# Performance work log

Measured on AMD Instinct MI355X. Metric: run time of the kernel, lower is better.

The kernel has to match this reference:

```python
import jax, jax.numpy as jnp
import numpy as np

B, S, HIDDEN = 2, 2048, 2048
NUM_HEADS, NUM_KV_HEADS, HEAD_DIM = 16, 4, 128
Q_SIZE = NUM_HEADS * HEAD_DIM          # 2048
KV_SIZE = NUM_KV_HEADS * HEAD_DIM      # 512
ROPE_THETA = 10000.0
NEG = -1e30


def setup_inputs() -> dict:
    key = jax.random.key(0)
    k1, k2, k3 = jax.random.split(key, 3)
    hidden_states = jax.random.normal(k1, (B, S, HIDDEN), jnp.float32)
    w_qkv = jax.random.normal(k2, (HIDDEN, Q_SIZE + 2 * KV_SIZE), jnp.float32) / np.sqrt(HIDDEN)
    w_o = jax.random.normal(k3, (Q_SIZE, HIDDEN), jnp.float32) / np.sqrt(Q_SIZE)
    positions = jnp.broadcast_to(jnp.arange(S, dtype=jnp.int32), (B, S))
    return {"positions": positions, "hidden_states": hidden_states,
            "w_qkv": w_qkv, "w_o": w_o}


def _rope(x, positions):
    # x: [B, S, H, D], neox-style rotate-half rope over full head_dim
    d = x.shape[-1]
    inv_freq = 1.0 / (ROPE_THETA ** (jnp.arange(0, d, 2, dtype=jnp.float32) / d))
    ang = positions[..., None].astype(jnp.float32) * inv_freq      # [B, S, D/2]
    cos = jnp.cos(ang)[:, :, None, :]
    sin = jnp.sin(ang)[:, :, None, :]
    x1, x2 = jnp.split(x, 2, axis=-1)
    return jnp.concatenate([x1 * cos - x2 * sin, x2 * cos + x1 * sin], axis=-1)


def reference(positions, hidden_states, w_qkv, w_o):
    qkv = jnp.einsum('bsh,ho->bso', hidden_states, w_qkv)
    q, k, v = jnp.split(qkv, [Q_SIZE, Q_SIZE + KV_SIZE], axis=-1)
    q = q.reshape(B, S, NUM_HEADS, HEAD_DIM)
    k = k.reshape(B, S, NUM_KV_HEADS, HEAD_DIM)
    v = v.reshape(B, S, NUM_KV_HEADS, HEAD_DIM)
    q = _rope(q, positions)
    k = _rope(k, positions)
    rep = NUM_HEADS // NUM_KV_HEADS
    k = jnp.repeat(k, rep, axis=2)   # GQA expand -> [B, S, NUM_HEADS, D]
    v = jnp.repeat(v, rep, axis=2)
    scale = HEAD_DIM ** -0.5
    scores = jnp.einsum('bqhd,bkhd->bhqk', q, k) * scale   # [B, H, S, S]
    causal = jnp.tril(jnp.ones((S, S), dtype=bool))
    scores = jnp.where(causal, scores, NEG)
    probs = jax.nn.softmax(scores, axis=-1)
    attn = jnp.einsum('bhqk,bkhd->bqhd', probs, v).reshape(B, S, Q_SIZE)
    return jnp.einsum('bsq,qh->bsh', attn, w_o)
```

## Files before the change

kernel.cpp:

```cpp
#include <hip/hip_runtime.h>
#include <hip/hip_bf16.h>
#include <stdint.h>

#define BDIM 2
#define SDIM 2048
#define HID 2048
#define NH 16
#define NKV 4
#define HD 128
#define QSZ 2048
#define KVSZ 512
#define QKVW 3072
#define TOK (BDIM*SDIM)

typedef __attribute__((ext_vector_type(8))) short bf16x8;
typedef __attribute__((ext_vector_type(4))) float f32x4;
typedef __attribute__((ext_vector_type(16))) float f32x16;

__device__ __forceinline__ short f2bf(float f) {
  return (short)__bfloat16_as_ushort(__float2bfloat16(f));
}

__device__ __forceinline__ float exp2_fast(float x) {
  float r;
  asm("v_exp_f32 %0, %1" : "=v"(r) : "v"(x));
  return r;
}

__device__ __forceinline__ void sincos_rev(float rev, float* sn, float* cs) {
  float fr, s, c;
  asm("v_fract_f32 %0, %1" : "=v"(fr) : "v"(rev));
  asm("v_sin_f32 %0, %1" : "=v"(s) : "v"(fr));
  asm("v_cos_f32 %0, %1" : "=v"(c) : "v"(fr));
  *sn = s; *cs = c;
}

__device__ __forceinline__ int xcd_swz(int orig, int nwg) {
  int cpx = nwg >> 3;
  return (orig & 7) * cpx + (orig >> 3);
}

__device__ __forceinline__ void gload_lds16(const void* g, void* lds) {
  __builtin_amdgcn_global_load_lds(
      (const __attribute__((address_space(1))) void*)g,
      (__attribute__((address_space(3))) void*)lds, 16, 0, 0);
}

__global__ __launch_bounds__(256) void k_prep(const float* __restrict__ hidden,
                                              const float* __restrict__ w_qkv,
                                              const float* __restrict__ w_o,
                                              short* __restrict__ X,
                                              short* __restrict__ WqkvT,
                                              short* __restrict__ WoT) {
  __shared__ short tile[64][65];
  const int bid = blockIdx.x;
  const int t = threadIdx.x;
  if (bid < 8192) {
    int i = (bid * 256 + t) * 4;
    float4 v = *(const float4*)(hidden + i);
    short4 o; o.x = f2bf(v.x); o.y = f2bf(v.y); o.z = f2bf(v.z); o.w = f2bf(v.w);
    *(short4*)(X + i) = o;
    return;
  }
  const float* in; short* out; int R, C, bx, by;
  if (bid < 9728) {
    int tt = bid - 8192; in = w_qkv; out = WqkvT; R = HID; C = QKVW;
    bx = tt % 48; by = tt / 48;
  } else {
    int tt = bid - 9728; in = w_o; out = WoT; R = QSZ; C = HID;
    bx = tt & 31; by = tt >> 5;
  }
  int k0 = by * 64, n0 = bx * 64;
#pragma unroll
  for (int i = 0; i < 16; ++i) {
    int idx = i * 256 + t;
    int kk = idx >> 6, nn = idx & 63;
    tile[kk][nn] = f2bf(in[(size_t)(k0 + kk) * C + n0 + nn]);
  }
  __syncthreads();
#pragma unroll
  for (int i = 0; i < 16; ++i) {
    int idx = i * 256 + t;
    int nn = idx >> 6, kk = idx & 63;
    out[(size_t)(n0 + nn) * R + k0 + kk] = tile[kk][nn];
  }
}

__global__ __launch_bounds__(256) void k_gemm_bf16(const short* __restrict__ A,
                                                   const short* __restrict__ Bt,
                                                   float* __restrict__ C,
                                                   int M, int N, int K) {
  __shared__ char lds[128 * 32 * 2 * 2];
  char* As = lds;
  char* Bs = lds + 8192;
  const int tid = threadIdx.x;
  const int w = tid >> 6, l = tid & 63;
  const int lq = l & 15, g = l >> 4;
  const int nx = N >> 7;
  const int bid = xcd_swz(blockIdx.x, nx * (M >> 7));
  const int m0 = (bid / nx) * 128, n0 = (bid % nx) * 128;
  const int wm = (w >> 1) * 64, wn = (w & 1) * 64;
  f32x4 acc[4][4] = {};

  const int nk = K >> 5;
  for (int kt = 0; kt < nk; ++kt) {
    const int k0 = kt * 32;
#pragma unroll
    for (int i = 0; i < 2; ++i) {
      int ch = (w + 4 * i) * 64 + l;
      int r = ch >> 2, cc = ch & 3;
      int gc = cc ^ ((r >> 1) & 3);
      gload_lds16(A + (size_t)(m0 + r) * K + k0 + gc * 8, As + (w + 4 * i) * 1024);
      gload_lds16(Bt + (size_t)(n0 + r) * K + k0 + gc * 8, Bs + (w + 4 * i) * 1024);
    }
    __syncthreads();
    bf16x8 af[4], bfr[4];
#pragma unroll
    for (int mi = 0; mi < 4; ++mi) {
      int row = wm + mi * 16 + lq;
      af[mi] = *(const bf16x8*)(As + row * 64 + ((g ^ ((row >> 1) & 3)) * 16));
    }
#pragma unroll
    for (int ni = 0; ni < 4; ++ni) {
      int row = wn + ni * 16 + lq;
      bfr[ni] = *(const bf16x8*)(Bs + row * 64 + ((g ^ ((row >> 1) & 3)) * 16));
    }
#pragma unroll
    for (int mi = 0; mi < 4; ++mi)
#pragma unroll
      for (int ni = 0; ni < 4; ++ni)
        acc[mi][ni] = __builtin_amdgcn_mfma_f32_16x16x32_bf16(af[mi], bfr[ni],
                                                              acc[mi][ni], 0, 0, 0);
    __syncthreads();
  }
#pragma unroll
  for (int mi = 0; mi < 4; ++mi)
#pragma unroll
    for (int ni = 0; ni < 4; ++ni)
#pragma unroll
      for (int r = 0; r < 4; ++r) {
        int row = m0 + wm + mi * 16 + 4 * g + r;
        int col = n0 + wn + ni * 16 + lq;
        C[(size_t)row * N + col] = acc[mi][ni][r];
      }
}

__global__ __launch_bounds__(256) void k_gemm_qkv_rope(const short* __restrict__ A,
                                                       const short* __restrict__ Bt,
                                                       const int* __restrict__ pos,
                                                       short* __restrict__ Qh,
                                                       short* __restrict__ Kh,
                                                       short* __restrict__ VT) {
  __shared__ char lds[128 * 32 * 2 * 2];
  char* As = lds;
  char* Bs = lds + 8192;
  const int tid = threadIdx.x;
  const int w = tid >> 6, l = tid & 63;
  const int lq = l & 15, g = l >> 4;
  const int bid = xcd_swz(blockIdx.x, (QKVW >> 7) * (TOK >> 7));
  const int hx = bid % (QKVW >> 7);
  const int m0 = (bid / (QKVW >> 7)) * 128, n0 = hx * 128;
  const int K = HID;
  f32x4 acc[2][8] = {};

  const int nk = K >> 5;
  for (int kt = 0; kt < nk; ++kt) {
    const int k0 = kt * 32;
#pragma unroll
    for (int i = 0; i < 2; ++i) {
      int ch = (w + 4 * i) * 64 + l;
      int r = ch >> 2, cc = ch & 3;
      int gc = cc ^ ((r >> 1) & 3);
      gload_lds16(A + (size_t)(m0 + r) * K + k0 + gc * 8, As + (w + 4 * i) * 1024);
      gload_lds16(Bt + (size_t)(n0 + r) * K + k0 + gc * 8, Bs + (w + 4 * i) * 1024);
    }
    __syncthreads();
    bf16x8 af[2], bfr[8];
#pragma unroll
    for (int mi = 0; mi < 2; ++mi) {
      int row = w * 32 + mi * 16 + lq;
      af[mi] = *(const bf16x8*)(As + row * 64 + ((g ^ ((row >> 1) & 3)) * 16));
    }
#pragma unroll
    for (int ni = 0; ni < 8; ++ni) {
      int row = ni * 16 + lq;
      bfr[ni] = *(const bf16x8*)(Bs + row * 64 + ((g ^ ((row >> 1) & 3)) * 16));
    }
#pragma unroll
    for (int mi = 0; mi < 2; ++mi)
#pragma unroll
      for (int ni = 0; ni < 8; ++ni)
        acc[mi][ni] = __builtin_amdgcn_mfma_f32_16x16x32_bf16(af[mi], bfr[ni],
                                                              acc[mi][ni], 0, 0, 0);
    __syncthreads();
  }

  const int b = m0 >> 11;
  if (hx < 20) {
    const float qscale = 0.12751743920f;
    const float sc = (hx < 16) ? qscale : 1.0f;
    short* dst = (hx < 16) ? (Qh + (size_t)(b * NH + hx) * SDIM * HD)
                           : (Kh + (size_t)(b * NKV + (hx - 16)) * SDIM * HD);
    float invf[4];
#pragma unroll
    for (int ni = 0; ni < 4; ++ni)
      invf[ni] = 0.15915494309f *
                 exp2_fast(-(float)(ni * 16 + lq) * (13.287712379549449f / 64.0f));
#pragma unroll
    for (int mi = 0; mi < 2; ++mi)
#pragma unroll
      for (int r = 0; r < 4; ++r) {
        int row = m0 + w * 32 + mi * 16 + 4 * g + r;
        int s = row & (SDIM - 1);
        float p = (float)pos[row];
        size_t hb = (size_t)s * HD;
#pragma unroll
        for (int ni = 0; ni < 4; ++ni) {
          float sn, cs;
          sincos_rev(p * invf[ni], &sn, &cs);
          float x1 = acc[mi][ni][r], x2 = acc[mi][ni + 4][r];
          dst[hb + ni * 16 + lq] = f2bf((x1 * cs - x2 * sn) * sc);
          dst[hb + ni * 16 + lq + 64] = f2bf((x2 * cs + x1 * sn) * sc);
        }
      }
  } else {
    const int hv = hx - 20;
    const int s00 = (m0 & (SDIM - 1)) + w * 32;
#pragma unroll
    for (int mi = 0; mi < 2; ++mi)
#pragma unroll
      for (int ni = 0; ni < 8; ++ni) {
        int d = ni * 16 + lq;
        int s0 = s00 + mi * 16 + 4 * g;
        size_t vb = ((size_t)(b * NKV + hv) * HD + d) * SDIM + s0;
        short4 ov;
        ov.x = f2bf(acc[mi][ni][0]); ov.y = f2bf(acc[mi][ni][1]);
        ov.z = f2bf(acc[mi][ni][2]); ov.w = f2bf(acc[mi][ni][3]);
        *(short4*)(VT + vb) = ov;
      }
  }
}

__global__ __launch_bounds__(256, 2) void k_attn(const short* __restrict__ Qh,
                                                 const short* __restrict__ Kh,
                                                 const short* __restrict__ VT,
                                                 short* __restrict__ attn, int S) {
  __shared__ char lds[2][32768];
  const int tid = threadIdx.x;
  const int w = tid >> 6, l = tid & 63;
  const int l31 = l & 31, hi = l >> 5;
  const int nqc = S / 128;
  const int bid = blockIdx.x;
  const int b = bid / (NH * nqc);
  const int rem = bid % (NH * nqc);
  const int h = rem / nqc;
  const int qc = nqc - 1 - (rem % nqc);
  const int q0 = qc * 128 + w * 32;
  const int kvh = h >> 2;
  const short* Qp = Qh + (size_t)(b * NH + h) * S * HD;
  const short* Kp = Kh + (size_t)(b * NKV + kvh) * S * HD;
  const short* Vp = VT + (size_t)(b * NKV + kvh) * HD * S;

  bf16x8 qf[8];
#pragma unroll
  for (int kc = 0; kc < 8; ++kc)
    qf[kc] = *(const bf16x8*)(Qp + (size_t)(q0 + l31) * HD + kc * 16 + hi * 8);

  f32x16 o[4] = {};
  float mrun = -1e30f, lrun = 0.f;
  const int qabs = q0 + l31;
  const int ntu = qc * 2 + 2;

#define STAGE(bufi, c0_)                                                          \
  {                                                                               \
    char* Kb = lds[bufi];                                                         \
    char* Vb = lds[bufi] + 16384;                                                 \
    _Pragma("unroll")                                                             \
    for (int i = 0; i < 4; ++i) {                                                 \
      int id = (i * 4 + w) * 64 + l;                                              \
      int kr = id >> 4, c16 = id & 15;                                            \
      gload_lds16(Kp + (size_t)((c0_) + kr) * HD + ((c16 ^ (kr & 15)) * 8),       \
                  Kb + (i * 4 + w) * 1024);                                       \
      int vr = id >> 3, c8 = id & 7;                                              \
      gload_lds16(Vp + (size_t)vr * S + (c0_) + ((c8 ^ (vr & 7)) * 8),            \
                  Vb + (i * 4 + w) * 1024);                                       \
    }                                                                             \
  }

  STAGE(0, 0);
  asm volatile("s_waitcnt vmcnt(0)" ::: "memory");
  __builtin_amdgcn_s_barrier();

  for (int c = 0; c < ntu; ++c) {
    const int c0 = c * 64;
    const int cur = c & 1;
    if (c + 1 < ntu) STAGE(cur ^ 1, c0 + 64);
    const char* Ks = lds[cur];
    const char* Vs = lds[cur] + 16384;

    f32x16 st[2];
    __builtin_amdgcn_s_setprio(1);
#pragma unroll
    for (int tt = 0; tt < 2; ++tt) {
      f32x16 s = {};
#pragma unroll
      for (int kc = 0; kc < 8; ++kc) {
        int kr = tt * 32 + l31;
        bf16x8 kf = *(const bf16x8*)(Ks + kr * 256 + (((kc * 2 + hi) ^ (l31 & 15)) * 16));
        s = __builtin_amdgcn_mfma_f32_32x32x16_bf16(kf, qf[kc], s, 0, 0, 0);
      }
      st[tt] = s;
    }
    __builtin_amdgcn_s_setprio(0);
    float tmax = -1e30f;
    if (c0 + 64 <= q0) {
#pragma unroll
      for (int tt = 0; tt < 2; ++tt)
#pragma unroll
        for (int r = 0; r < 16; ++r) tmax = fmaxf(tmax, st[tt][r]);
    } else {
#pragma unroll
      for (int tt = 0; tt < 2; ++tt)
#pragma unroll
        for (int r = 0; r < 16; ++r) {
          int kv = c0 + tt * 32 + (r & 3) + 8 * (r >> 2) + 4 * hi;
          float sv = (kv <= qabs) ? st[tt][r] : -1e30f;
          st[tt][r] = sv;
          tmax = fmaxf(tmax, sv);
        }
    }
    tmax = fmaxf(tmax, __shfl_xor(tmax, 32));
    if (!__all(tmax - mrun <= 8.0f)) {
      float mnew = fmaxf(mrun, tmax);
      float fac = exp2_fast(mrun - mnew);
      lrun *= fac;
#pragma unroll
      for (int d0 = 0; d0 < 4; ++d0) o[d0] = o[d0] * fac;
      mrun = mnew;
    }
    float sum = 0.f;
#pragma unroll
    for (int tt = 0; tt < 2; ++tt)
#pragma unroll
      for (int r = 0; r < 16; ++r) {
        float e = exp2_fast(st[tt][r] - mrun);
        st[tt][r] = e;
        sum += e;
      }
    sum += __shfl_xor(sum, 32);
    lrun += sum;
    __builtin_amdgcn_s_setprio(1);
#pragma unroll
    for (int j = 0; j < 4; ++j) {
      const int tt = j >> 1, kc = j & 1;
      uint32_t W0 = (uint32_t)(uint16_t)f2bf(st[tt][8 * kc + 0]) |
                    ((uint32_t)(uint16_t)f2bf(st[tt][8 * kc + 1]) << 16);
      uint32_t W1 = (uint32_t)(uint16_t)f2bf(st[tt][8 * kc + 2]) |
                    ((uint32_t)(uint16_t)f2bf(st[tt][8 * kc + 3]) << 16);
      uint32_t W2 = (uint32_t)(uint16_t)f2bf(st[tt][8 * kc + 4]) |
                    ((uint32_t)(uint16_t)f2bf(st[tt][8 * kc + 5]) << 16);
      uint32_t W3 = (uint32_t)(uint16_t)f2bf(st[tt][8 * kc + 6]) |
                    ((uint32_t)(uint16_t)f2bf(st[tt][8 * kc + 7]) << 16);
      uint32_t Y0 = __shfl_xor(hi ? W0 : W2, 32);
      uint32_t Y1 = __shfl_xor(hi ? W1 : W3, 32);
      union { uint32_t u[4]; bf16x8 v; } pu;
      pu.u[0] = hi ? Y0 : W0;
      pu.u[1] = hi ? Y1 : W1;
      pu.u[2] = hi ? W2 : Y0;
      pu.u[3] = hi ? W3 : Y1;
#pragma unroll
      for (int d0 = 0; d0 < 4; ++d0) {
        int vr = d0 * 32 + l31;
        bf16x8 vf = *(const bf16x8*)(Vs + vr * 128 + (((j * 2 + hi) ^ (vr & 7)) * 16));
        o[d0] = __builtin_amdgcn_mfma_f32_32x32x16_bf16(vf, pu.v, o[d0], 0, 0, 0);
      }
    }
    __builtin_amdgcn_s_setprio(0);
    asm volatile("s_waitcnt vmcnt(0)" ::: "memory");
    __builtin_amdgcn_s_barrier();
  }
#undef STAGE
  float inv = 1.0f / lrun;
  size_t rowb = (size_t)(b * S + q0 + l31) * QSZ + h * HD;
#pragma unroll
  for (int d0 = 0; d0 < 4; ++d0)
#pragma unroll
    for (int gq = 0; gq < 4; ++gq) {
      short4 ov;
      ov.x = f2bf(o[d0][4 * gq + 0] * inv);
      ov.y = f2bf(o[d0][4 * gq + 1] * inv);
      ov.z = f2bf(o[d0][4 * gq + 2] * inv);
      ov.w = f2bf(o[d0][4 * gq + 3] * inv);
      *(short4*)(attn + rowb + d0 * 32 + 8 * gq + 4 * hi) = ov;
    }
}

extern "C" void kernel_launch(void* const* d_in, const int* in_sizes, int n_in,
                              void* d_out, int out_size, void* d_ws, size_t ws_size,
                              hipStream_t stream) {
  const int* positions = (const int*)d_in[0];
  const float* hidden = (const float*)d_in[1];
  const float* w_qkv = (const float*)d_in[2];
  const float* w_o = (const float*)d_in[3];
  float* out = (float*)d_out;

  char* ws = (char*)d_ws;
  short* X     = (short*)(ws);
  short* WqkvT = (short*)(ws + 16777216);
  short* WoT   = (short*)(ws + 29360128);
  short* Qh    = (short*)(ws + 88080384);
  short* Kh    = (short*)(ws + 104857600);
  short* VT    = (short*)(ws + 109051904);
  short* ATT   = (short*)(ws + 113246208);

  k_prep<<<10752, 256, 0, stream>>>(hidden, w_qkv, w_o, X, WqkvT, WoT);
  k_gemm_qkv_rope<<<(QKVW / 128) * (TOK / 128), 256, 0, stream>>>(X, WqkvT, positions,
                                                                  Qh, Kh, VT);
  k_attn<<<BDIM * NH * (SDIM / 128), 256, 0, stream>>>(Qh, Kh, VT, ATT, SDIM);
  k_gemm_bf16<<<(HID / 128) * (TOK / 128), 256, 0, stream>>>(ATT, WoT, out, TOK, HID, QSZ);
}
```

Measured before the change: 217.6 us.

## Restructure attention so one block serves four GQA heads with 16x16 MFMA tiles

Each attention block now handles one KV head and 16 query rows, with its four waves covering the four query heads that share that KV head, so each staged K/V tile is reused across heads. The kernel moves from 32x32x16 to 16x16x32 MFMA, uses 32-key chunks with smaller LDS buffers, and passes P through a per-wave LDS scratch instead of cross-lane shuffles. Launch bounds rise to 4 blocks per CU and the grid doubles. In exchange, each block covers fewer query rows, so K/V traffic per query and the number of barriers per key grow.

New measurement: 234.1 us. +7.6%, slower.

```diff
diff --git a/kernel.cpp b/kernel.cpp
--- a/kernel.cpp
+++ b/kernel.cpp
@@ -241,48 +241,50 @@
   }
 }
 
-__global__ __launch_bounds__(256, 2) void k_attn(const short* __restrict__ Qh,
+__global__ __launch_bounds__(256, 4) void k_attn(const short* __restrict__ Qh,
                                                  const short* __restrict__ Kh,
                                                  const short* __restrict__ VT,
                                                  short* __restrict__ attn, int S) {
-  __shared__ char lds[2][32768];
+  __shared__ char lds[2][16384];
+  __shared__ __align__(16) char plds[4][1280];
   const int tid = threadIdx.x;
   const int w = tid >> 6, l = tid & 63;
-  const int l31 = l & 31, hi = l >> 5;
-  const int nqc = S / 128;
+  const int lq = l & 15, g = l >> 4;
+  const int ntc = S / 16;
   const int bid = blockIdx.x;
-  const int b = bid / (NH * nqc);
-  const int rem = bid % (NH * nqc);
-  const int h = rem / nqc;
-  const int qc = nqc - 1 - (rem % nqc);
-  const int q0 = qc * 128 + w * 32;
-  const int kvh = h >> 2;
+  const int b = bid / (NKV * ntc);
+  const int rem = bid % (NKV * ntc);
+  const int kvh = rem / ntc;
+  const int tc = ntc - 1 - (rem % ntc);
+  const int q0 = tc * 16;
+  const int h = kvh * 4 + w;
   const short* Qp = Qh + (size_t)(b * NH + h) * S * HD;
   const short* Kp = Kh + (size_t)(b * NKV + kvh) * S * HD;
   const short* Vp = VT + (size_t)(b * NKV + kvh) * HD * S;
-
-  bf16x8 qf[8];
-#pragma unroll
-  for (int kc = 0; kc < 8; ++kc)
-    qf[kc] = *(const bf16x8*)(Qp + (size_t)(q0 + l31) * HD + kc * 16 + hi * 8);
-
-  f32x16 o[4] = {};
+  char* Pw = plds[w];
+
+  bf16x8 qf[4];
+#pragma unroll
+  for (int kc = 0; kc < 4; ++kc)
+    qf[kc] = *(const bf16x8*)(Qp + (size_t)(q0 + lq) * HD + kc * 32 + g * 8);
+
+  f32x4 o[8] = {};
   float mrun = -1e30f, lrun = 0.f;
-  const int qabs = q0 + l31;
-  const int ntu = qc * 2 + 2;
+  const int qabs = q0 + lq;
+  const int ntu = (q0 >> 5) + 1;
 
 #define STAGE(bufi, c0_)                                                          \
   {                                                                               \
     char* Kb = lds[bufi];                                                         \
-    char* Vb = lds[bufi] + 16384;                                                 \
+    char* Vb = lds[bufi] + 8192;                                                  \
     _Pragma("unroll")                                                             \
-    for (int i = 0; i < 4; ++i) {                                                 \
+    for (int i = 0; i < 2; ++i) {                                                 \
       int id = (i * 4 + w) * 64 + l;                                              \
       int kr = id >> 4, c16 = id & 15;                                            \
       gload_lds16(Kp + (size_t)((c0_) + kr) * HD + ((c16 ^ (kr & 15)) * 8),       \
                   Kb + (i * 4 + w) * 1024);                                       \
-      int vr = id >> 3, c8 = id & 7;                                              \
-      gload_lds16(Vp + (size_t)vr * S + (c0_) + ((c8 ^ (vr & 7)) * 8),            \
+      int vr = id >> 2, c4 = id & 3;                                              \
+      gload_lds16(Vp + (size_t)vr * S + (c0_) + ((c4 ^ ((vr >> 1) & 3)) * 8),     \
                   Vb + (i * 4 + w) * 1024);                                       \
     }                                                                             \
   }
@@ -292,88 +294,84 @@
   __builtin_amdgcn_s_barrier();
 
   for (int c = 0; c < ntu; ++c) {
-    const int c0 = c * 64;
+    const int c0 = c * 32;
     const int cur = c & 1;
-    if (c + 1 < ntu) STAGE(cur ^ 1, c0 + 64);
+    if (c + 1 < ntu) STAGE(cur ^ 1, c0 + 32);
     const char* Ks = lds[cur];
-    const char* Vs = lds[cur] + 16384;
-
-    f32x16 st[2];
+    const char* Vs = lds[cur] + 8192;
+
+    f32x4 st[2] = {};
     __builtin_amdgcn_s_setprio(1);
 #pragma unroll
-    for (int tt = 0; tt < 2; ++tt) {
-      f32x16 s = {};
-#pragma unroll
-      for (int kc = 0; kc < 8; ++kc) {
-        int kr = tt * 32 + l31;
-        bf16x8 kf = *(const bf16x8*)(Ks + kr * 256 + (((kc * 2 + hi) ^ (l31 & 15)) * 16));
-        s = __builtin_amdgcn_mfma_f32_32x32x16_bf16(kf, qf[kc], s, 0, 0, 0);
+    for (int t16 = 0; t16 < 2; ++t16) {
+      int kr = t16 * 16 + lq;
+#pragma unroll
+      for (int kc = 0; kc < 4; ++kc) {
+        bf16x8 kf = *(const bf16x8*)(Ks + kr * 256 + (((kc * 4 + g) ^ (kr & 15)) * 16));
+        st[t16] = __builtin_amdgcn_mfma_f32_16x16x32_bf16(kf, qf[kc], st[t16], 0, 0, 0);
       }
-      st[tt] = s;
     }
     __builtin_amdgcn_s_setprio(0);
     float tmax = -1e30f;
-    if (c0 + 64 <= q0) {
-#pragma unroll
-      for (int tt = 0; tt < 2; ++tt)
-#pragma unroll
-        for (int r = 0; r < 16; ++r) tmax = fmaxf(tmax, st[tt][r]);
+    if (c0 + 32 <= q0) {
+#pragma unroll
+      for (int t16 = 0; t16 < 2; ++t16)
+#pragma unroll
+        for (int r = 0; r < 4; ++r) tmax = fmaxf(tmax, st[t16][r]);
     } else {
 #pragma unroll
-      for (int tt = 0; tt < 2; ++tt)
-#pragma unroll
-        for (int r = 0; r < 16; ++r) {
-          int kv = c0 + tt * 32 + (r & 3) + 8 * (r >> 2) + 4 * hi;
-          float sv = (kv <= qabs) ? st[tt][r] : -1e30f;
-          st[tt][r] = sv;
+      for (int t16 = 0; t16 < 2; ++t16)
+#pragma unroll
+        for (int r = 0; r < 4; ++r) {
+          int kv = c0 + t16 * 16 + 4 * g + r;
+          float sv = (kv <= qabs) ? st[t16][r] : -1e30f;
+          st[t16][r] = sv;
           tmax = fmaxf(tmax, sv);
         }
     }
+    tmax = fmaxf(tmax, __shfl_xor(tmax, 16));
     tmax = fmaxf(tmax, __shfl_xor(tmax, 32));
     if (!__all(tmax - mrun <= 8.0f)) {
       float mnew = fmaxf(mrun, tmax);
       float fac = exp2_fast(mrun - mnew);
       lrun *= fac;
 #pragma unroll
-      for (int d0 = 0; d0 < 4; ++d0) o[d0] = o[d0] * fac;
+      for (int d0 = 0; d0 < 8; ++d0) o[d0] = o[d0] * fac;
       mrun = mnew;
     }
     float sum = 0.f;
 #pragma unroll
-    for (int tt = 0; tt < 2; ++tt)
-#pragma unroll
-      for (int r = 0; r < 16; ++r) {
-        float e = exp2_fast(st[tt][r] - mrun);
-        st[tt][r] = e;
+    for (int t16 = 0; t16 < 2; ++t16)
+#pragma unroll
+      for (int r = 0; r < 4; ++r) {
+        float e = exp2_fast(st[t16][r] - mrun);
+        st[t16][r] = e;
         sum += e;
       }
+    sum += __shfl_xor(sum, 16);
     sum += __shfl_xor(sum, 32);
     lrun += sum;
+    {
+      uint32_t a0 = (uint32_t)(uint16_t)f2bf(st[0][0]) |
+                    ((uint32_t)(uint16_t)f2bf(st[0][1]) << 16);
+      uint32_t a1 = (uint32_t)(uint16_t)f2bf(st[0][2]) |
+                    ((uint32_t)(uint16_t)f2bf(st[0][3]) << 16);
+      uint32_t b0 = (uint32_t)(uint16_t)f2bf(st[1][0]) |
+                    ((uint32_t)(uint16_t)f2bf(st[1][1]) << 16);
+      uint32_t b1 = (uint32_t)(uint16_t)f2bf(st[1][2]) |
+                    ((uint32_t)(uint16_t)f2bf(st[1][3]) << 16);
+      uint2 pa; pa.x = a0; pa.y = a1;
+      uint2 pb2; pb2.x = b0; pb2.y = b1;
+      *(uint2*)(Pw + lq * 80 + g * 8) = pa;
+      *(uint2*)(Pw + lq * 80 + 32 + g * 8) = pb2;
+    }
+    bf16x8 pb = *(const bf16x8*)(Pw + lq * 80 + g * 16);
     __builtin_amdgcn_s_setprio(1);
 #pragma unroll
-    for (int j = 0; j < 4; ++j) {
-      const int tt = j >> 1, kc = j & 1;
-      uint32_t W0 = (uint32_t)(uint16_t)f2bf(st[tt][8 * kc + 0]) |
-                    ((uint32_t)(uint16_t)f2bf(st[tt][8 * kc + 1]) << 16);
-      uint32_t W1 = (uint32_t)(uint16_t)f2bf(st[tt][8 * kc + 2]) |
-                    ((uint32_t)(uint16_t)f2bf(st[tt][8 * kc + 3]) << 16);
-      uint32_t W2 = (uint32_t)(uint16_t)f2bf(st[tt][8 * kc + 4]) |
-                    ((uint32_t)(uint16_t)f2bf(st[tt][8 * kc + 5]) << 16);
-      uint32_t W3 = (uint32_t)(uint16_t)f2bf(st[tt][8 * kc + 6]) |
-                    ((uint32_t)(uint16_t)f2bf(st[tt][8 * kc + 7]) << 16);
-      uint32_t Y0 = __shfl_xor(hi ? W0 : W2, 32);
-      uint32_t Y1 = __shfl_xor(hi ? W1 : W3, 32);
-      union { uint32_t u[4]; bf16x8 v; } pu;
-      pu.u[0] = hi ? Y0 : W0;
-      pu.u[1] = hi ? Y1 : W1;
-      pu.u[2] = hi ? W2 : Y0;
-      pu.u[3] = hi ? W3 : Y1;
-#pragma unroll
-      for (int d0 = 0; d0 < 4; ++d0) {
-        int vr = d0 * 32 + l31;
-        bf16x8 vf = *(const bf16x8*)(Vs + vr * 128 + (((j * 2 + hi) ^ (vr & 7)) * 16));
-        o[d0] = __builtin_amdgcn_mfma_f32_32x32x16_bf16(vf, pu.v, o[d0], 0, 0, 0);
-      }
+    for (int d0 = 0; d0 < 8; ++d0) {
+      int vr = d0 * 16 + lq;
+      bf16x8 vf = *(const bf16x8*)(Vs + vr * 64 + (((g ^ ((vr >> 1) & 3))) * 16));
+      o[d0] = __builtin_amdgcn_mfma_f32_16x16x32_bf16(vf, pb, o[d0], 0, 0, 0);
     }
     __builtin_amdgcn_s_setprio(0);
     asm volatile("s_waitcnt vmcnt(0)" ::: "memory");
@@ -381,18 +379,16 @@
   }
 #undef STAGE
   float inv = 1.0f / lrun;
-  size_t rowb = (size_t)(b * S + q0 + l31) * QSZ + h * HD;
-#pragma unroll
-  for (int d0 = 0; d0 < 4; ++d0)
-#pragma unroll
-    for (int gq = 0; gq < 4; ++gq) {
-      short4 ov;
-      ov.x = f2bf(o[d0][4 * gq + 0] * inv);
-      ov.y = f2bf(o[d0][4 * gq + 1] * inv);
-      ov.z = f2bf(o[d0][4 * gq + 2] * inv);
-      ov.w = f2bf(o[d0][4 * gq + 3] * inv);
-      *(short4*)(attn + rowb + d0 * 32 + 8 * gq + 4 * hi) = ov;
-    }
+  size_t rowb = (size_t)(b * S + q0 + lq) * QSZ + h * HD;
+#pragma unroll
+  for (int d0 = 0; d0 < 8; ++d0) {
+    short4 ov;
+    ov.x = f2bf(o[d0][0] * inv);
+    ov.y = f2bf(o[d0][1] * inv);
+    ov.z = f2bf(o[d0][2] * inv);
+    ov.w = f2bf(o[d0][3] * inv);
+    *(short4*)(attn + rowb + d0 * 16 + 4 * g) = ov;
+  }
 }
 
 extern "C" void kernel_launch(void* const* d_in, const int* in_sizes, int n_in,
@@ -416,6 +412,6 @@
   k_prep<<<10752, 256, 0, stream>>>(hidden, w_qkv, w_o, X, WqkvT, WoT);
   k_gemm_qkv_rope<<<(QKVW / 128) * (TOK / 128), 256, 0, stream>>>(X, WqkvT, positions,
                                                                   Qh, Kh, VT);
-  k_attn<<<BDIM * NH * (SDIM / 128), 256, 0, stream>>>(Qh, Kh, VT, ATT, SDIM);
+  k_attn<<<BDIM * NKV * (SDIM / 16), 256, 0, stream>>>(Qh, Kh, VT, ATT, SDIM);
   k_gemm_bf16<<<(HID / 128) * (TOK / 128), 256, 0, stream>>>(ATT, WoT, out, TOK, HID, QSZ);
 }
```
